# Optimization experiments

Hardware: AMD Instinct MI355X
Metric: run time of the kernel (lower is better)

The kernel has to match this reference:

```python
import jax, jax.numpy as jnp
import numpy as np

B, R, C, H, W = 8, 4, 64, 128, 128
RF, E = 256, 8
C2 = 2 * C
K = 3


def setup_inputs() -> dict:
    key = jax.random.key(0)
    ks = jax.random.split(key, 8)
    return {
        "x": jax.random.normal(ks[0], (B, C, H, W), jnp.float32),
        "routing": jax.random.normal(ks[1], (B, R, RF), jnp.float32),
        # nn.Linear(routing_features, num_experts)
        "routing_W": jax.random.normal(ks[2], (RF, E), jnp.float32) * 0.05,
        "routing_b": jnp.zeros((E,), jnp.float32),
        # CondConv2d expert weights: (E, Cout, Cin, k, k)
        "W1": jax.random.normal(ks[3], (E, C2, C, K, K), jnp.float32) * 0.04,
        "prelu_a": jnp.float32(0.25),  # PReLU single shared parameter
        "W2": jax.random.normal(ks[4], (E, C, C2, K, K), jnp.float32) * 0.03,
        # self-routing Linear(2*in_features, num_experts)
        "sr_W": jax.random.normal(ks[5], (C2, E), jnp.float32) * 0.08,
        "sr_b": jnp.zeros((E,), jnp.float32),
        # conv_output: Conv2d(in_features, 1, kernel_size=1) with bias
        "Wout": jax.random.normal(ks[6], (1, C), jnp.float32) * 0.1,
        "bout": jnp.zeros((1,), jnp.float32),
    }


def _prelu(x, a):
    return jnp.where(x >= 0, x, a * x)


def _cond_conv(x, rw, Wexp):
    # x: (B,Cin,H,W); rw: (B,E); Wexp: (E,Cout,Cin,k,k)
    # per-sample mixed kernel, then per-sample conv (vmap over batch)
    w = jnp.einsum('be,eoikl->boikl', rw, Wexp)
    def one(xi, wi):
        return jax.lax.conv_general_dilated(
            xi[None], wi, window_strides=(1, 1), padding=[(1, 1), (1, 1)])[0]
    return jax.vmap(one)(x, w)


def reference(x, routing, routing_W, routing_b, W1, prelu_a, W2, sr_W, sr_b, Wout, bout):
    rw = jax.nn.sigmoid(routing @ routing_W + routing_b)  # (B,R,E)
    rw = jnp.transpose(rw, (1, 0, 2))                     # (R,B,E)

    def per_head(rw_r):
        xc = _prelu(_cond_conv(x, rw_r, W1), prelu_a)      # (B,C2,H,W)
        pooled = xc.mean(axis=(2, 3))                      # adaptive_avg_pool2d(.,1)
        srw = pooled @ sr_W + sr_b                         # no sigmoid (per source)
        xc2 = _prelu(_cond_conv(xc, srw, W2), prelu_a)     # (B,C,H,W)
        out = jnp.einsum('bchw,oc->bohw', xc2, Wout)       # 1x1 conv
        return out + bout[None, :, None, None]             # (B,1,H,W)

    res = jax.vmap(per_head)(rw)                           # (R,B,1,H,W)
    return jnp.transpose(res[:, :, 0], (1, 0, 2, 3))       # (B,R,H,W)
```

## Files before the change

### kernel.cpp

```cpp
#include <hip/hip_runtime.h>
#include <stdint.h>


typedef _Float16 f16_t;
typedef _Float16 f16x8 __attribute__((ext_vector_type(8)));
typedef _Float16 f16x4 __attribute__((ext_vector_type(4)));
typedef float    f32x4 __attribute__((ext_vector_type(4)));

#define B_   8
#define R_   4
#define C_   64
#define C2_  128
#define H_   128
#define W_   128
#define E_   8
#define RF_  256
#define WP_  130
#define HP_  130

__device__ __forceinline__ f32x4 mfma16(f16x8 a, f16x8 b, f32x4 c) {
  return __builtin_amdgcn_mfma_f32_16x16x32_f16(a, b, c, 0, 0, 0);
}

__device__ __forceinline__ void gl16(const f16_t* g, f16_t* l) {
  __builtin_amdgcn_global_load_lds(
      (const __attribute__((address_space(1))) unsigned int*)(const void*)g,
      (__attribute__((address_space(3))) unsigned int*)(void*)l, 16, 0, 0);
}

__device__ __host__ __forceinline__ int sig(int n) { return (n ^ (n >> 2)) & 3; }

__global__ void k_rw(const float* __restrict__ routing, const float* __restrict__ rW,
                     const float* __restrict__ rB, float* __restrict__ rw,
                     float* __restrict__ pooled4) {
  int t = threadIdx.x;
  #pragma unroll
  for (int i = 0; i < 16; ++i) pooled4[i*256 + t] = 0.f;
  int e = t & 7, b = (t >> 3) & 7, r = t >> 6;
  float acc = rB[e];
  for (int f = 0; f < RF_; ++f)
    acc += routing[(b*R_ + r)*RF_ + f] * rW[f*E_ + e];
  rw[(r*B_ + b)*E_ + e] = 1.0f / (1.0f + __expf(-acc));
}

__global__ void k_zero(f16_t* __restrict__ xbt, f16_t* __restrict__ xct,
                       size_t xct_stride) {
  const f16x8 z = {0,0,0,0,0,0,0,0};
  int t = blockIdx.x*256 + threadIdx.x;
  if (t < 16640) {
    int ch = t & 7, u = t >> 3;
    int pix = u % 130; u /= 130;
    int rs = u & 1, b = u >> 1;
    *(f16x8*)&xbt[((size_t)(b*HP_ + rs*129)*WP_ + pix)*C_ + ch*8] = z;
    return;
  }
  t -= 16640;
  if (t < 133120) {
    int ch = t & 15, u = t >> 4;
    int pix = u % 130; u /= 130;
    int rs = u & 1; u >>= 1;
    int b = u & 7, r = u >> 3;
    *(f16x8*)&xct[(size_t)r*xct_stride + ((size_t)(b*HP_ + rs*129)*WP_ + pix)*C2_ + ch*8] = z;
    return;
  }
  t -= 133120;
  if (t < 131072) {
    int ch = t & 15, u = t >> 4;
    int hp = (u & 127) + 1; u >>= 7;
    int cs = u & 1; u >>= 1;
    int b = u & 7, r = u >> 3;
    *(f16x8*)&xct[(size_t)r*xct_stride + ((size_t)(b*HP_ + hp)*WP_ + cs*129)*C2_ + ch*8] = z;
  }
}

__global__ void k_xt(const float* __restrict__ x, f16_t* __restrict__ xbt) {
  int wh = blockIdx.x, h = blockIdx.y, b = blockIdx.z;
  int t = threadIdx.x;
  int w0 = wh * 64;
  __shared__ float tile[64][65];
  #pragma unroll
  for (int rep = 0; rep < 16; ++rep) {
    int idx = rep*256 + t;
    int c = idx >> 6, w = idx & 63;
    tile[c][w] = x[((size_t)(b*C_ + c)*H_ + h)*W_ + w0 + w];
  }
  __syncthreads();
  #pragma unroll
  for (int rep = 0; rep < 16; ++rep) {
    int idx = rep*256 + t;
    int w = idx >> 6, c = idx & 63;
    xbt[((size_t)(b*HP_ + h + 1)*WP_ + (w0 + w + 1))*C_ + c] = (f16_t)tile[c][w];
  }
  if (t < 64) {
    if (wh == 0) xbt[((size_t)(b*HP_ + h + 1)*WP_ + 0)*C_ + t]   = (f16_t)0.0f;
    else         xbt[((size_t)(b*HP_ + h + 1)*WP_ + 129)*C_ + t] = (f16_t)0.0f;
  }
}

__global__ void k_mix1(const float* __restrict__ rw, const float* __restrict__ W1,
                       f16_t* __restrict__ w1m) {
  int gid = blockIdx.x*256 + threadIdx.x;
  int cq4 = gid & 15;
  int s   = (gid >> 4) % 9;
  int t2  = (gid >> 4) / 9;
  int co  = t2 & 127;
  int rb  = t2 >> 7;
  float o0=0.f,o1=0.f,o2=0.f,o3=0.f;
  #pragma unroll
  for (int e = 0; e < E_; ++e) {
    float rv = rw[rb*E_ + e];
    const float* wp = W1 + (size_t)((e*C2_ + co)*C_ + cq4*4)*9 + s;
    o0 += rv*wp[0]; o1 += rv*wp[9]; o2 += rv*wp[18]; o3 += rv*wp[27];
  }
  f16x4 pk; pk[0]=(f16_t)o0; pk[1]=(f16_t)o1; pk[2]=(f16_t)o2; pk[3]=(f16_t)o3;
  int coh = co >> 6, co6 = co & 63;
  int cb  = cq4 >> 3;
  int cqu = (cq4 >> 1) & 3;
  int off = (cq4 & 1) * 4;
  size_t row = ((size_t)(rb*2 + coh)*2 + cb)*64 + co6;
  *(f16x4*)&w1m[row*288 + (size_t)(s*4 + (cqu ^ sig(co6)))*8 + off] = pk;
}

__global__ void k_mix2(const float* __restrict__ pooled, const float* __restrict__ srW,
                       const float* __restrict__ srb, const float* __restrict__ W2,
                       f16_t* __restrict__ w2m, size_t w2m_stride, int r0) {
  const int r = r0 + blockIdx.y;
  const float* pooled_r = pooled + (size_t)r*B_*C2_;
  f16_t* w2m_r = w2m + (size_t)r*w2m_stride;
  __shared__ float sw[64];
  int t = threadIdx.x;
  if (t < 64) {
    int b = t >> 3, e = t & 7;
    float acc = srb[e];
    for (int c = 0; c < C2_; ++c)
      acc += pooled_r[b*C2_ + c] * (1.0f/16384.0f) * srW[c*E_ + e];
    sw[t] = acc;
  }
  __syncthreads();
  int gid = blockIdx.x*256 + t;
  int c2q = gid & 31;
  int s   = (gid >> 5) % 9;
  int t2  = (gid >> 5) / 9;
  int co  = t2 & 63;
  int b   = t2 >> 6;
  float o0=0.f,o1=0.f,o2=0.f,o3=0.f;
  #pragma unroll
  for (int e = 0; e < E_; ++e) {
    float rv = sw[b*E_ + e];
    const float* wp = W2 + (size_t)((e*C_ + co)*C2_ + c2q*4)*9 + s;
    o0 += rv*wp[0]; o1 += rv*wp[9]; o2 += rv*wp[18]; o3 += rv*wp[27];
  }
  f16x4 pk; pk[0]=(f16_t)o0; pk[1]=(f16_t)o1; pk[2]=(f16_t)o2; pk[3]=(f16_t)o3;
  int it  = c2q >> 3;
  int cqu = (c2q >> 1) & 3;
  int off = (c2q & 1) * 4;
  size_t row = ((size_t)b*4 + it)*64 + co;
  *(f16x4*)&w2m_r[row*288 + (size_t)(s*4 + (cqu ^ sig(co)))*8 + off] = pk;
}

__global__ __launch_bounds__(256, 2) void k_conv1(
    const f16_t* __restrict__ xbt, const f16_t* __restrict__ w1m,
    const float* __restrict__ pa, f16_t* __restrict__ xct, size_t xct_stride,
    float* __restrict__ pooled, int r0)
{
  const int bx = blockIdx.x;
  const int b = bx & 7, h0 = (bx >> 3) << 1;
  const int coh = blockIdx.y;
  const int r = r0 + blockIdx.z;
  f16_t* xct_r = xct + (size_t)r*xct_stride;
  float* pooled_r = pooled + (size_t)r*B_*C2_;
  const int tid = threadIdx.x;
  const int lane = tid & 63;
  const int wid = tid >> 6;
  const int wrow = wid >> 1, wph = wid & 1;
  const int l15 = lane & 15, l4 = lane >> 4;
  __shared__ __align__(16) f16_t lA[64*288];
  __shared__ __align__(16) f16_t lB[2080*8];

  const int xorA = (l4 ^ sig(l15)) << 4;
  int bbase[3];
  #pragma unroll
  for (int dw = 0; dw < 3; ++dw) {
    int P0 = wph*64 + dw + l15;
    bbase[dw] = P0*64 + ((l4 ^ sig(P0)) << 4);
  }

  const f32x4 vzero = {0.f,0.f,0.f,0.f};
  f32x4 acc[4][4];
  #pragma unroll
  for (int i=0;i<4;++i)
    #pragma unroll
    for (int j=0;j<4;++j) acc[i][j] = vzero;

  const int rb = r*B_ + b;
  const f16_t* w1base = w1m + ((size_t)(rb*2 + coh)*2)*64*288;
  const f16_t* xb = xbt + ((size_t)(b*HP_ + h0))*WP_*C_;

  for (int cb = 0; cb < 2; ++cb) {
    __syncthreads();
    #pragma unroll
    for (int k = 0; k < 9; ++k) {
      int u = k*256 + tid;
      gl16(w1base + (size_t)cb*64*288 + (size_t)u*8, &lA[u*8]);
    }
    #pragma unroll
    for (int k = 0; k < 8; ++k) {
      int u = k*256 + tid;
      int row = u / 520, rem = u - row*520;
      int pix = rem >> 2, cq = (rem & 3) ^ sig(pix);
      gl16(xb + ((size_t)row*WP_ + pix)*C_ + cb*32 + cq*8, &lB[u*8]);
    }
    if (tid < 32) {
      int u = 2048 + tid;
      int rem = u - 1560;
      int pix = rem >> 2, cq = (rem & 3) ^ sig(pix);
      gl16(xb + ((size_t)3*WP_ + pix)*C_ + cb*32 + cq*8, &lB[u*8]);
    }
    __syncthreads();
    __builtin_amdgcn_s_setprio(1);
    #pragma unroll
    for (int dh = 0; dh < 3; ++dh) {
      #pragma unroll
      for (int dw = 0; dw < 3; ++dw) {
        const int s = dh*3 + dw;
        f16x8 af[4], bf[4];
        #pragma unroll
        for (int fm = 0; fm < 4; ++fm)
          af[fm] = *(const f16x8*)((const char*)lA + (fm*16 + l15)*576 + s*64 + xorA);
        #pragma unroll
        for (int fn = 0; fn < 4; ++fn)
          bf[fn] = *(const f16x8*)((const char*)lB + (wrow + dh)*8320 + bbase[dw] + fn*1024);
        #pragma unroll
        for (int fm = 0; fm < 4; ++fm)
          #pragma unroll
          for (int fn = 0; fn < 4; ++fn)
            acc[fm][fn] = mfma16(af[fm], bf[fn], acc[fm][fn]);
      }
    }
    __builtin_amdgcn_s_setprio(0);
  }

  const float a = pa[0];
  float ps[4][4];
  #pragma unroll
  for (int fm=0;fm<4;++fm)
    #pragma unroll
    for (int j=0;j<4;++j) ps[fm][j] = 0.f;
  #pragma unroll
  for (int fm = 0; fm < 4; ++fm)
    #pragma unroll
    for (int fn = 0; fn < 4; ++fn)
      #pragma unroll
      for (int j = 0; j < 4; ++j) {
        float v = acc[fm][fn][j];
        v = (v >= 0.f) ? v : a*v;
        acc[fm][fn][j] = v;
        ps[fm][j] += v;
      }
  #pragma unroll
  for (int fm = 0; fm < 4; ++fm)
    #pragma unroll
    for (int j = 0; j < 4; ++j) {
      float s = ps[fm][j];
      s += __shfl_xor(s, 1, 64);
      s += __shfl_xor(s, 2, 64);
      s += __shfl_xor(s, 4, 64);
      s += __shfl_xor(s, 8, 64);
      ps[fm][j] = s;
    }
  __syncthreads();
  f16_t* lso = lA;
  float* lps = (float*)lB;
  const int prow = wrow*128 + wph*64;
  #pragma unroll
  for (int fm = 0; fm < 4; ++fm)
    #pragma unroll
    for (int fn = 0; fn < 4; ++fn) {
      f16x4 pk;
      #pragma unroll
      for (int j = 0; j < 4; ++j) pk[j] = (f16_t)acc[fm][fn][j];
      *(f16x4*)&lso[(prow + fn*16 + l15)*72 + fm*16 + l4*4] = pk;
    }
  if (l15 == 0) {
    #pragma unroll
    for (int fm = 0; fm < 4; ++fm)
      #pragma unroll
      for (int j = 0; j < 4; ++j)
        lps[wid*64 + fm*16 + l4*4 + j] = ps[fm][j];
  }
  __syncthreads();
  #pragma unroll
  for (int p = 0; p < 8; ++p) {
    int i = p*256 + tid;
    int pl = i >> 3, q = i & 7;
    int row = pl >> 7, pix = pl & 127;
    uint4 v = *(const uint4*)&lso[pl*72 + q*8];
    *(uint4*)(xct_r + ((size_t)(b*HP_ + h0 + row + 1)*WP_ + pix + 1)*C2_ + coh*64 + q*8) = v;
  }
  if (tid < 64) {
    float s = lps[tid] + lps[64 + tid] + lps[128 + tid] + lps[192 + tid];
    atomicAdd(&pooled_r[b*C2_ + coh*64 + tid], s);
  }
}

__global__ __launch_bounds__(256, 2) void k_conv2(
    const f16_t* __restrict__ xct, size_t xct_stride,
    const f16_t* __restrict__ w2m, size_t w2m_stride,
    const float* __restrict__ pa, const float* __restrict__ Wout,
    const float* __restrict__ bout, float* __restrict__ out, int r0)
{
  const int bx = blockIdx.x;
  const int b = bx & 7, h0 = (bx >> 3) << 1;
  const int r = r0 + blockIdx.y;
  const int tid = threadIdx.x;
  const int lane = tid & 63;
  const int wid = tid >> 6;
  const int wrow = wid >> 1, wph = wid & 1;
  const int l15 = lane & 15, l4 = lane >> 4;
  __shared__ __align__(16) f16_t lA[64*288];
  __shared__ __align__(16) f16_t lB[2080*8];

  const int xorA = (l4 ^ sig(l15)) << 4;
  int bbase[3];
  #pragma unroll
  for (int dw = 0; dw < 3; ++dw) {
    int P0 = wph*64 + dw + l15;
    bbase[dw] = P0*64 + ((l4 ^ sig(P0)) << 4);
  }

  const f32x4 vzero = {0.f,0.f,0.f,0.f};
  f32x4 acc[4][4];
  #pragma unroll
  for (int i=0;i<4;++i)
    #pragma unroll
    for (int j=0;j<4;++j) acc[i][j] = vzero;

  const f16_t* w2base = w2m + (size_t)r*w2m_stride + (size_t)b*4*64*288;
  const f16_t* xb = xct + (size_t)r*xct_stride + ((size_t)(b*HP_ + h0))*WP_*C2_;

  for (int it = 0; it < 4; ++it) {
    __syncthreads();
    #pragma unroll
    for (int k = 0; k < 9; ++k) {
      int u = k*256 + tid;
      gl16(w2base + (size_t)it*64*288 + (size_t)u*8, &lA[u*8]);
    }
    #pragma unroll
    for (int k = 0; k < 8; ++k) {
      int u = k*256 + tid;
      int row = u / 520, rem = u - row*520;
      int pix = rem >> 2, cq = (rem & 3) ^ sig(pix);
      gl16(xb + ((size_t)row*WP_ + pix)*C2_ + it*32 + cq*8, &lB[u*8]);
    }
    if (tid < 32) {
      int u = 2048 + tid;
      int rem = u - 1560;
      int pix = rem >> 2, cq = (rem & 3) ^ sig(pix);
      gl16(xb + ((size_t)3*WP_ + pix)*C2_ + it*32 + cq*8, &lB[u*8]);
    }
    __syncthreads();
    __builtin_amdgcn_s_setprio(1);
    #pragma unroll
    for (int dh = 0; dh < 3; ++dh) {
      #pragma unroll
      for (int dw = 0; dw < 3; ++dw) {
        const int s = dh*3 + dw;
        f16x8 af[4], bf[4];
        #pragma unroll
        for (int fm = 0; fm < 4; ++fm)
          af[fm] = *(const f16x8*)((const char*)lA + (fm*16 + l15)*576 + s*64 + xorA);
        #pragma unroll
        for (int fn = 0; fn < 4; ++fn)
          bf[fn] = *(const f16x8*)((const char*)lB + (wrow + dh)*8320 + bbase[dw] + fn*1024);
        #pragma unroll
        for (int fm = 0; fm < 4; ++fm)
          #pragma unroll
          for (int fn = 0; fn < 4; ++fn)
            acc[fm][fn] = mfma16(af[fm], bf[fn], acc[fm][fn]);
      }
    }
    __builtin_amdgcn_s_setprio(0);
  }

  const float a  = pa[0];
  const float bo = bout[0];
  float wr_[4][4];
  #pragma unroll
  for (int fm = 0; fm < 4; ++fm)
    #pragma unroll
    for (int j = 0; j < 4; ++j)
      wr_[fm][j] = Wout[fm*16 + l4*4 + j];
  float* orow = out + ((size_t)((b*R_ + r)*H_ + h0 + wrow))*W_;
  #pragma unroll
  for (int fn = 0; fn < 4; ++fn) {
    float s = 0.f;
    #pragma unroll
    for (int fm = 0; fm < 4; ++fm)
      #pragma unroll
      for (int j = 0; j < 4; ++j) {
        float v = acc[fm][fn][j];
        v = (v >= 0.f) ? v : a*v;
        s += wr_[fm][j]*v;
      }
    s += __shfl_xor(s, 16, 64);
    s += __shfl_xor(s, 32, 64);
    if (lane < 16)
      orow[wph*64 + fn*16 + lane] = s + bo;
  }
}

extern "C" void kernel_launch(void* const* d_in, const int* in_sizes, int n_in,
                              void* d_out, int out_size, void* d_ws, size_t ws_size,
                              hipStream_t stream) {
  (void)in_sizes; (void)n_in; (void)out_size;
  const float* x       = (const float*)d_in[0];
  const float* routing = (const float*)d_in[1];
  const float* rW      = (const float*)d_in[2];
  const float* rB      = (const float*)d_in[3];
  const float* W1      = (const float*)d_in[4];
  const float* pa      = (const float*)d_in[5];
  const float* W2      = (const float*)d_in[6];
  const float* srW     = (const float*)d_in[7];
  const float* srb     = (const float*)d_in[8];
  const float* Wout    = (const float*)d_in[9];
  const float* bout    = (const float*)d_in[10];
  float* out = (float*)d_out;

  const size_t xct_one = (size_t)B_*HP_*WP_*C2_;
  const size_t w2m_one = (size_t)2048*288;
  const size_t need_fused = 17305600ull + 4718592ull + 4*xct_one*2 + 4*w2m_one*2 + 32768ull;
  const bool fused = (ws_size >= need_fused);
  const int ncopies = fused ? 4 : 1;
  const size_t xs = fused ? xct_one : 0;
  const size_t ws2 = fused ? w2m_one : 0;

  char* ws = (char*)d_ws;
  size_t off = 0;
  f16_t* xbt = (f16_t*)(ws + off); off += (size_t)B_*HP_*WP_*C_*2;
  f16_t* w1m = (f16_t*)(ws + off); off += (size_t)8192*288*2;
  f16_t* xct = (f16_t*)(ws + off); off += xct_one*2*ncopies;
  f16_t* w2m = (f16_t*)(ws + off); off += w2m_one*2*ncopies;
  float* rw     = (float*)(ws + off); off += (size_t)R_*B_*E_*4;
  float* pooled = (float*)(ws + off); off += (size_t)R_*B_*C2_*4;

  k_rw  <<<1, 256, 0, stream>>>(routing, rW, rB, rw, pooled);
  k_zero<<<1097, 256, 0, stream>>>(xbt, xct, xs);
  k_xt  <<<dim3(2, H_, B_), 256, 0, stream>>>(x, xbt);
  k_mix1<<<2304, 256, 0, stream>>>(rw, W1, w1m);
  if (fused) {
    k_conv1<<<dim3(512, 2, 4), 256, 0, stream>>>(xbt, w1m, pa, xct, xs, pooled, 0);
    k_mix2 <<<dim3(576, 4), 256, 0, stream>>>(pooled, srW, srb, W2, w2m, ws2, 0);
    k_conv2<<<dim3(512, 4), 256, 0, stream>>>(xct, xs, w2m, ws2, pa, Wout, bout, out, 0);
  } else {
    for (int r = 0; r < R_; ++r) {
      k_conv1<<<dim3(512, 2, 1), 256, 0, stream>>>(xbt, w1m, pa, xct, xs, pooled, r);
      k_mix2 <<<dim3(576, 1), 256, 0, stream>>>(pooled, srW, srb, W2, w2m, ws2, r);
      k_conv2<<<dim3(512, 1), 256, 0, stream>>>(xct, xs, w2m, ws2, pa, Wout, bout, out, r);
    }
  }
}
```

Before: 242.8 us.

## Switch activations to channel-group-planar layout and enlarge conv tiles to 8 rows

Activations and mixed weights now use an 8-channel-unit, channel-group-major layout instead of pixel-major with an XOR swizzle. Each conv block covers 8 output rows with 512 threads, so the haloed input tile is reused across more rows. Weights are streamed per tap into a double buffer that is prefetched while the MFMAs run, and conv2 prefetches the next channel block into registers. The cost is a barrier after every tap, larger LDS use that limits occupancy, more pooled atomics, and a serialized staged store of the conv1 output.

```diff
diff --git a/kernel.cpp b/kernel.cpp
--- a/kernel.cpp
+++ b/kernel.cpp
@@ -15,8 +15,8 @@
 #define W_   128
 #define E_   8
 #define RF_  256
+#define HP_  130
 #define WP_  130
-#define HP_  130
 
 __device__ __forceinline__ f32x4 mfma16(f16x8 a, f16x8 b, f32x4 c) {
   return __builtin_amdgcn_mfma_f32_16x16x32_f16(a, b, c, 0, 0, 0);
@@ -27,8 +27,6 @@
       (const __attribute__((address_space(1))) unsigned int*)(const void*)g,
       (__attribute__((address_space(3))) unsigned int*)(void*)l, 16, 0, 0);
 }
-
-__device__ __host__ __forceinline__ int sig(int n) { return (n ^ (n >> 2)) & 3; }
 
 __global__ void k_rw(const float* __restrict__ routing, const float* __restrict__ rW,
                      const float* __restrict__ rB, float* __restrict__ rw,
@@ -44,32 +42,27 @@
 }
 
 __global__ void k_zero(f16_t* __restrict__ xbt, f16_t* __restrict__ xct,
-                       size_t xct_stride) {
+                       size_t xsu) {
   const f16x8 z = {0,0,0,0,0,0,0,0};
   int t = blockIdx.x*256 + threadIdx.x;
   if (t < 16640) {
-    int ch = t & 7, u = t >> 3;
-    int pix = u % 130; u /= 130;
-    int rs = u & 1, b = u >> 1;
-    *(f16x8*)&xbt[((size_t)(b*HP_ + rs*129)*WP_ + pix)*C_ + ch*8] = z;
+    int un = t % 1040, q = t / 1040;
+    int rs = q & 1, b = q >> 1;
+    *(f16x8*)&xbt[((size_t)(b*HP_ + rs*129)*1040 + un)*8] = z;
     return;
   }
   t -= 16640;
   if (t < 133120) {
-    int ch = t & 15, u = t >> 4;
-    int pix = u % 130; u /= 130;
-    int rs = u & 1; u >>= 1;
-    int b = u & 7, r = u >> 3;
-    *(f16x8*)&xct[(size_t)r*xct_stride + ((size_t)(b*HP_ + rs*129)*WP_ + pix)*C2_ + ch*8] = z;
+    int un = t % 2080, q = t / 2080;
+    int rs = q & 1, b = (q >> 1) & 7, r = q >> 4;
+    *(f16x8*)&xct[((size_t)r*xsu + (size_t)(b*HP_ + rs*129)*2080 + un)*8] = z;
     return;
   }
   t -= 133120;
   if (t < 131072) {
-    int ch = t & 15, u = t >> 4;
-    int hp = (u & 127) + 1; u >>= 7;
-    int cs = u & 1; u >>= 1;
-    int b = u & 7, r = u >> 3;
-    *(f16x8*)&xct[(size_t)r*xct_stride + ((size_t)(b*HP_ + hp)*WP_ + cs*129)*C2_ + ch*8] = z;
+    int cs = t & 1, u = (t >> 1) & 15, prow = ((t >> 5) & 127) + 1;
+    int b = (t >> 12) & 7, r = t >> 15;
+    *(f16x8*)&xct[((size_t)r*xsu + (size_t)(b*HP_ + prow)*2080 + u*130 + cs*129)*8] = z;
   }
 }
 
@@ -85,15 +78,17 @@
     tile[c][w] = x[((size_t)(b*C_ + c)*H_ + h)*W_ + w0 + w];
   }
   __syncthreads();
+  size_t rowb = (size_t)(b*HP_ + h + 1)*1040;
   #pragma unroll
   for (int rep = 0; rep < 16; ++rep) {
     int idx = rep*256 + t;
     int w = idx >> 6, c = idx & 63;
-    xbt[((size_t)(b*HP_ + h + 1)*WP_ + (w0 + w + 1))*C_ + c] = (f16_t)tile[c][w];
+    xbt[(rowb + (c>>3)*130 + (w0 + w + 1))*8 + (c & 7)] = (f16_t)tile[c][w];
   }
   if (t < 64) {
-    if (wh == 0) xbt[((size_t)(b*HP_ + h + 1)*WP_ + 0)*C_ + t]   = (f16_t)0.0f;
-    else         xbt[((size_t)(b*HP_ + h + 1)*WP_ + 129)*C_ + t] = (f16_t)0.0f;
+    int u = t >> 3, c7 = t & 7;
+    int gp = (wh == 0) ? 0 : 129;
+    xbt[(rowb + u*130 + gp)*8 + c7] = (f16_t)0.0f;
   }
 }
 
@@ -114,19 +109,17 @@
   }
   f16x4 pk; pk[0]=(f16_t)o0; pk[1]=(f16_t)o1; pk[2]=(f16_t)o2; pk[3]=(f16_t)o3;
   int coh = co >> 6, co6 = co & 63;
-  int cb  = cq4 >> 3;
-  int cqu = (cq4 >> 1) & 3;
-  int off = (cq4 & 1) * 4;
-  size_t row = ((size_t)(rb*2 + coh)*2 + cb)*64 + co6;
-  *(f16x4*)&w1m[row*288 + (size_t)(s*4 + (cqu ^ sig(co6)))*8 + off] = pk;
+  int cb = cq4 >> 3, u2 = (cq4 >> 1) & 3, half = cq4 & 1;
+  size_t unit = ((size_t)(((rb*2 + coh)*2 + cb)*9 + s)*4 + u2)*64 + co6;
+  *(f16x4*)&w1m[unit*8 + half*4] = pk;
 }
 
 __global__ void k_mix2(const float* __restrict__ pooled, const float* __restrict__ srW,
                        const float* __restrict__ srb, const float* __restrict__ W2,
-                       f16_t* __restrict__ w2m, size_t w2m_stride, int r0) {
+                       f16_t* __restrict__ w2m, int r0) {
   const int r = r0 + blockIdx.y;
   const float* pooled_r = pooled + (size_t)r*B_*C2_;
-  f16_t* w2m_r = w2m + (size_t)r*w2m_stride;
+  f16_t* w2m_r = w2m + (size_t)r*73728*8;
   __shared__ float sw[64];
   int t = threadIdx.x;
   if (t < 64) {
@@ -151,93 +144,87 @@
     o0 += rv*wp[0]; o1 += rv*wp[9]; o2 += rv*wp[18]; o3 += rv*wp[27];
   }
   f16x4 pk; pk[0]=(f16_t)o0; pk[1]=(f16_t)o1; pk[2]=(f16_t)o2; pk[3]=(f16_t)o3;
-  int it  = c2q >> 3;
-  int cqu = (c2q >> 1) & 3;
-  int off = (c2q & 1) * 4;
-  size_t row = ((size_t)b*4 + it)*64 + co;
-  *(f16x4*)&w2m_r[row*288 + (size_t)(s*4 + (cqu ^ sig(co)))*8 + off] = pk;
-}
-
-__global__ __launch_bounds__(256, 2) void k_conv1(
+  int cb = c2q >> 3, u2 = (c2q >> 1) & 3, half = c2q & 1;
+  size_t unit = ((size_t)((b*4 + cb)*9 + s)*4 + u2)*64 + co;
+  *(f16x4*)&w2m_r[unit*8 + half*4] = pk;
+}
+
+__global__ __launch_bounds__(512, 2) void k_conv1(
     const f16_t* __restrict__ xbt, const f16_t* __restrict__ w1m,
-    const float* __restrict__ pa, f16_t* __restrict__ xct, size_t xct_stride,
+    const float* __restrict__ pa, f16_t* __restrict__ xct, size_t xsu,
     float* __restrict__ pooled, int r0)
 {
   const int bx = blockIdx.x;
-  const int b = bx & 7, h0 = (bx >> 3) << 1;
+  const int b = bx & 7, h0 = (bx >> 3) << 3;
   const int coh = blockIdx.y;
   const int r = r0 + blockIdx.z;
-  f16_t* xct_r = xct + (size_t)r*xct_stride;
-  float* pooled_r = pooled + (size_t)r*B_*C2_;
   const int tid = threadIdx.x;
   const int lane = tid & 63;
   const int wid = tid >> 6;
-  const int wrow = wid >> 1, wph = wid & 1;
   const int l15 = lane & 15, l4 = lane >> 4;
-  __shared__ __align__(16) f16_t lA[64*288];
-  __shared__ __align__(16) f16_t lB[2080*8];
-
-  const int xorA = (l4 ^ sig(l15)) << 4;
-  int bbase[3];
-  #pragma unroll
-  for (int dw = 0; dw < 3; ++dw) {
-    int P0 = wph*64 + dw + l15;
-    bbase[dw] = P0*64 + ((l4 ^ sig(P0)) << 4);
-  }
-
-  const f32x4 vzero = {0.f,0.f,0.f,0.f};
-  f32x4 acc[4][4];
+  __shared__ __align__(16) f16_t lB[5200*8];
+  __shared__ __align__(16) f16_t lA[2][256*8];
+
+  f32x4 acc[4][8];
   #pragma unroll
   for (int i=0;i<4;++i)
     #pragma unroll
-    for (int j=0;j<4;++j) acc[i][j] = vzero;
-
-  const int rb = r*B_ + b;
-  const f16_t* w1base = w1m + ((size_t)(rb*2 + coh)*2)*64*288;
-  const f16_t* xb = xbt + ((size_t)(b*HP_ + h0))*WP_*C_;
-
+    for (int j=0;j<8;++j) acc[i][j] = (f32x4){0.f,0.f,0.f,0.f};
+
+  const f16_t* xsrc  = xbt + ((size_t)(b*HP_ + h0))*1040*8;
+  const f16_t* wbase = w1m + ((size_t)((r*B_ + b)*2 + coh))*2*9*256*8;
+  f16_t* xct_r = xct + (size_t)blockIdx.z*xsu*8;
+
+  #pragma unroll
+  for (int k = 0; k < 10; ++k) {
+    int u = tid + 512*k; int lr = u/520, j = u - lr*520;
+    gl16(xsrc + ((size_t)(lr*1040 + j))*8, &lB[u*8]);
+  }
+  if (tid < 80) {
+    int u = 5120 + tid; int lr = u/520, j = u - lr*520;
+    gl16(xsrc + ((size_t)(lr*1040 + j))*8, &lB[u*8]);
+  }
+  if (tid < 256) gl16(wbase + (size_t)tid*8, &lA[0][tid*8]);
+  __syncthreads();
+
+  int cur = 0;
   for (int cb = 0; cb < 2; ++cb) {
-    __syncthreads();
-    #pragma unroll
-    for (int k = 0; k < 9; ++k) {
-      int u = k*256 + tid;
-      gl16(w1base + (size_t)cb*64*288 + (size_t)u*8, &lA[u*8]);
-    }
-    #pragma unroll
-    for (int k = 0; k < 8; ++k) {
-      int u = k*256 + tid;
-      int row = u / 520, rem = u - row*520;
-      int pix = rem >> 2, cq = (rem & 3) ^ sig(pix);
-      gl16(xb + ((size_t)row*WP_ + pix)*C_ + cb*32 + cq*8, &lB[u*8]);
-    }
-    if (tid < 32) {
-      int u = 2048 + tid;
-      int rem = u - 1560;
-      int pix = rem >> 2, cq = (rem & 3) ^ sig(pix);
-      gl16(xb + ((size_t)3*WP_ + pix)*C_ + cb*32 + cq*8, &lB[u*8]);
-    }
-    __syncthreads();
-    __builtin_amdgcn_s_setprio(1);
-    #pragma unroll
-    for (int dh = 0; dh < 3; ++dh) {
-      #pragma unroll
-      for (int dw = 0; dw < 3; ++dw) {
-        const int s = dh*3 + dw;
-        f16x8 af[4], bf[4];
+    if (cb) {
+      #pragma unroll
+      for (int k = 0; k < 10; ++k) {
+        int u = tid + 512*k; int lr = u/520, j = u - lr*520;
+        gl16(xsrc + ((size_t)(lr*1040 + 520 + j))*8, &lB[u*8]);
+      }
+      if (tid < 80) {
+        int u = 5120 + tid; int lr = u/520, j = u - lr*520;
+        gl16(xsrc + ((size_t)(lr*1040 + 520 + j))*8, &lB[u*8]);
+      }
+      __syncthreads();
+    }
+    #pragma unroll
+    for (int s = 0; s < 9; ++s) {
+      const int nc = (s < 8) ? cb : cb + 1;
+      const int ns = (s < 8) ? s + 1 : 0;
+      if (nc < 2 && tid < 256)
+        gl16(wbase + ((size_t)((nc*9 + ns)*256 + tid))*8, &lA[cur^1][tid*8]);
+      const int dh = s / 3, dw = s % 3;
+      f16x8 af[4], bf[8];
+      #pragma unroll
+      for (int fm = 0; fm < 4; ++fm)
+        af[fm] = *(const f16x8*)&lA[cur][(l4*64 + fm*16 + l15)*8];
+      #pragma unroll
+      for (int fn = 0; fn < 8; ++fn)
+        bf[fn] = *(const f16x8*)&lB[((wid + dh)*520 + l4*130 + fn*16 + l15 + dw)*8];
+      __builtin_amdgcn_s_setprio(1);
+      #pragma unroll
+      for (int fm = 0; fm < 4; ++fm)
         #pragma unroll
-        for (int fm = 0; fm < 4; ++fm)
-          af[fm] = *(const f16x8*)((const char*)lA + (fm*16 + l15)*576 + s*64 + xorA);
-        #pragma unroll
-        for (int fn = 0; fn < 4; ++fn)
-          bf[fn] = *(const f16x8*)((const char*)lB + (wrow + dh)*8320 + bbase[dw] + fn*1024);
-        #pragma unroll
-        for (int fm = 0; fm < 4; ++fm)
-          #pragma unroll
-          for (int fn = 0; fn < 4; ++fn)
-            acc[fm][fn] = mfma16(af[fm], bf[fn], acc[fm][fn]);
-      }
-    }
-    __builtin_amdgcn_s_setprio(0);
+        for (int fn = 0; fn < 8; ++fn)
+          acc[fm][fn] = mfma16(af[fm], bf[fn], acc[fm][fn]);
+      __builtin_amdgcn_s_setprio(0);
+      __syncthreads();
+      cur ^= 1;
+    }
   }
 
   const float a = pa[0];
@@ -249,7 +236,7 @@
   #pragma unroll
   for (int fm = 0; fm < 4; ++fm)
     #pragma unroll
-    for (int fn = 0; fn < 4; ++fn)
+    for (int fn = 0; fn < 8; ++fn)
       #pragma unroll
       for (int j = 0; j < 4; ++j) {
         float v = acc[fm][fn][j];
@@ -266,120 +253,119 @@
       s += __shfl_xor(s, 2, 64);
       s += __shfl_xor(s, 4, 64);
       s += __shfl_xor(s, 8, 64);
-      ps[fm][j] = s;
-    }
-  __syncthreads();
-  f16_t* lso = lA;
-  float* lps = (float*)lB;
-  const int prow = wrow*128 + wph*64;
-  #pragma unroll
-  for (int fm = 0; fm < 4; ++fm)
-    #pragma unroll
-    for (int fn = 0; fn < 4; ++fn) {
-      f16x4 pk;
-      #pragma unroll
-      for (int j = 0; j < 4; ++j) pk[j] = (f16_t)acc[fm][fn][j];
-      *(f16x4*)&lso[(prow + fn*16 + l15)*72 + fm*16 + l4*4] = pk;
-    }
-  if (l15 == 0) {
-    #pragma unroll
-    for (int fm = 0; fm < 4; ++fm)
-      #pragma unroll
-      for (int j = 0; j < 4; ++j)
-        lps[wid*64 + fm*16 + l4*4 + j] = ps[fm][j];
-  }
-  __syncthreads();
-  #pragma unroll
-  for (int p = 0; p < 8; ++p) {
-    int i = p*256 + tid;
-    int pl = i >> 3, q = i & 7;
-    int row = pl >> 7, pix = pl & 127;
-    uint4 v = *(const uint4*)&lso[pl*72 + q*8];
-    *(uint4*)(xct_r + ((size_t)(b*HP_ + h0 + row + 1)*WP_ + pix + 1)*C2_ + coh*64 + q*8) = v;
-  }
-  if (tid < 64) {
-    float s = lps[tid] + lps[64 + tid] + lps[128 + tid] + lps[192 + tid];
-    atomicAdd(&pooled_r[b*C2_ + coh*64 + tid], s);
-  }
-}
-
-__global__ __launch_bounds__(256, 2) void k_conv2(
-    const f16_t* __restrict__ xct, size_t xct_stride,
-    const f16_t* __restrict__ w2m, size_t w2m_stride,
+      if (l15 == 0)
+        atomicAdd(&pooled[(size_t)r*B_*C2_ + b*C2_ + coh*64 + fm*16 + l4*4 + j], s);
+    }
+  #pragma unroll
+  for (int t4 = 0; t4 < 4; ++t4) {
+    if ((wid >> 1) == t4) {
+      const int rr = wid & 1;
+      #pragma unroll
+      for (int fm = 0; fm < 4; ++fm)
+        #pragma unroll
+        for (int fn = 0; fn < 8; ++fn) {
+          f16x4 pk;
+          #pragma unroll
+          for (int j = 0; j < 4; ++j) pk[j] = (f16_t)acc[fm][fn][j];
+          int pix = fn*16 + l15;
+          int cof = (fm*16 + l4*4) ^ ((pix & 7) << 3);
+          *(f16x4*)&lB[(rr*128 + pix)*64 + cof] = pk;
+        }
+    }
+    __syncthreads();
+    #pragma unroll
+    for (int k = 0; k < 4; ++k) {
+      int idx = tid + 512*k;
+      int rr = idx >> 10, u = (idx >> 7) & 7, pix = idx & 127;
+      f16x8 v = *(const f16x8*)&lB[(rr*128 + pix)*64 + ((u ^ (pix & 7)) << 3)];
+      size_t gu = (size_t)(b*HP_ + h0 + 2*t4 + rr + 1)*2080 + (coh*8 + u)*130 + pix + 1;
+      *(f16x8*)(xct_r + gu*8) = v;
+    }
+    __syncthreads();
+  }
+}
+
+__global__ __launch_bounds__(512, 2) void k_conv2(
+    const f16_t* __restrict__ xct, size_t xsu,
+    const f16_t* __restrict__ w2m,
     const float* __restrict__ pa, const float* __restrict__ Wout,
     const float* __restrict__ bout, float* __restrict__ out, int r0)
 {
   const int bx = blockIdx.x;
-  const int b = bx & 7, h0 = (bx >> 3) << 1;
+  const int b = bx & 7, h0 = (bx >> 3) << 3;
   const int r = r0 + blockIdx.y;
   const int tid = threadIdx.x;
   const int lane = tid & 63;
   const int wid = tid >> 6;
-  const int wrow = wid >> 1, wph = wid & 1;
   const int l15 = lane & 15, l4 = lane >> 4;
-  __shared__ __align__(16) f16_t lA[64*288];
-  __shared__ __align__(16) f16_t lB[2080*8];
-
-  const int xorA = (l4 ^ sig(l15)) << 4;
-  int bbase[3];
-  #pragma unroll
-  for (int dw = 0; dw < 3; ++dw) {
-    int P0 = wph*64 + dw + l15;
-    bbase[dw] = P0*64 + ((l4 ^ sig(P0)) << 4);
-  }
-
-  const f32x4 vzero = {0.f,0.f,0.f,0.f};
-  f32x4 acc[4][4];
+  __shared__ __align__(16) f16_t lB[5200*8];
+  __shared__ __align__(16) f16_t lA[2][256*8];
+
+  f32x4 acc[4][8];
   #pragma unroll
   for (int i=0;i<4;++i)
     #pragma unroll
-    for (int j=0;j<4;++j) acc[i][j] = vzero;
-
-  const f16_t* w2base = w2m + (size_t)r*w2m_stride + (size_t)b*4*64*288;
-  const f16_t* xb = xct + (size_t)r*xct_stride + ((size_t)(b*HP_ + h0))*WP_*C2_;
-
-  for (int it = 0; it < 4; ++it) {
-    __syncthreads();
-    #pragma unroll
-    for (int k = 0; k < 9; ++k) {
-      int u = k*256 + tid;
-      gl16(w2base + (size_t)it*64*288 + (size_t)u*8, &lA[u*8]);
-    }
-    #pragma unroll
-    for (int k = 0; k < 8; ++k) {
-      int u = k*256 + tid;
-      int row = u / 520, rem = u - row*520;
-      int pix = rem >> 2, cq = (rem & 3) ^ sig(pix);
-      gl16(xb + ((size_t)row*WP_ + pix)*C2_ + it*32 + cq*8, &lB[u*8]);
-    }
-    if (tid < 32) {
-      int u = 2048 + tid;
-      int rem = u - 1560;
-      int pix = rem >> 2, cq = (rem & 3) ^ sig(pix);
-      gl16(xb + ((size_t)3*WP_ + pix)*C2_ + it*32 + cq*8, &lB[u*8]);
-    }
-    __syncthreads();
-    __builtin_amdgcn_s_setprio(1);
-    #pragma unroll
-    for (int dh = 0; dh < 3; ++dh) {
-      #pragma unroll
-      for (int dw = 0; dw < 3; ++dw) {
-        const int s = dh*3 + dw;
-        f16x8 af[4], bf[4];
+    for (int j=0;j<8;++j) acc[i][j] = (f32x4){0.f,0.f,0.f,0.f};
+
+  const f16_t* xsrc  = xct + ((size_t)blockIdx.y*xsu + (size_t)(b*HP_ + h0)*2080)*8;
+  const f16_t* wbase = w2m + ((size_t)r*73728 + (size_t)b*4*9*256)*8;
+
+  #pragma unroll
+  for (int k = 0; k < 10; ++k) {
+    int u = tid + 512*k; int lr = u/520, j = u - lr*520;
+    gl16(xsrc + ((size_t)(lr*2080 + j))*8, &lB[u*8]);
+  }
+  if (tid < 80) {
+    int u = 5120 + tid; int lr = u/520, j = u - lr*520;
+    gl16(xsrc + ((size_t)(lr*2080 + j))*8, &lB[u*8]);
+  }
+  if (tid < 256) gl16(wbase + (size_t)tid*8, &lA[0][tid*8]);
+  __syncthreads();
+
+  int cur = 0;
+  uint4 br[11];
+  for (int cb = 0; cb < 4; ++cb) {
+    if (cb < 3) {
+      #pragma unroll
+      for (int k = 0; k < 10; ++k) {
+        int u = tid + 512*k; int lr = u/520, j = u - lr*520;
+        br[k] = *(const uint4*)(xsrc + ((size_t)(lr*2080 + (cb+1)*520 + j))*8);
+      }
+      if (tid < 80) {
+        int u = 5120 + tid; int lr = u/520, j = u - lr*520;
+        br[10] = *(const uint4*)(xsrc + ((size_t)(lr*2080 + (cb+1)*520 + j))*8);
+      }
+    }
+    #pragma unroll
+    for (int s = 0; s < 9; ++s) {
+      const int nc = (s < 8) ? cb : cb + 1;
+      const int ns = (s < 8) ? s + 1 : 0;
+      if (nc < 4 && tid < 256)
+        gl16(wbase + ((size_t)((nc*9 + ns)*256 + tid))*8, &lA[cur^1][tid*8]);
+      const int dh = s / 3, dw = s % 3;
+      f16x8 af[4], bf[8];
+      #pragma unroll
+      for (int fm = 0; fm < 4; ++fm)
+        af[fm] = *(const f16x8*)&lA[cur][(l4*64 + fm*16 + l15)*8];
+      #pragma unroll
+      for (int fn = 0; fn < 8; ++fn)
+        bf[fn] = *(const f16x8*)&lB[((wid + dh)*520 + l4*130 + fn*16 + l15 + dw)*8];
+      __builtin_amdgcn_s_setprio(1);
+      #pragma unroll
+      for (int fm = 0; fm < 4; ++fm)
         #pragma unroll
-        for (int fm = 0; fm < 4; ++fm)
-          af[fm] = *(const f16x8*)((const char*)lA + (fm*16 + l15)*576 + s*64 + xorA);
-        #pragma unroll
-        for (int fn = 0; fn < 4; ++fn)
-          bf[fn] = *(const f16x8*)((const char*)lB + (wrow + dh)*8320 + bbase[dw] + fn*1024);
-        #pragma unroll
-        for (int fm = 0; fm < 4; ++fm)
-          #pragma unroll
-          for (int fn = 0; fn < 4; ++fn)
-            acc[fm][fn] = mfma16(af[fm], bf[fn], acc[fm][fn]);
-      }
-    }
-    __builtin_amdgcn_s_setprio(0);
+        for (int fn = 0; fn < 8; ++fn)
+          acc[fm][fn] = mfma16(af[fm], bf[fn], acc[fm][fn]);
+      __builtin_amdgcn_s_setprio(0);
+      __syncthreads();
+      cur ^= 1;
+    }
+    if (cb < 3) {
+      #pragma unroll
+      for (int k = 0; k < 10; ++k) { int u = tid + 512*k; *(uint4*)&lB[u*8] = br[k]; }
+      if (tid < 80)                { int u = 5120 + tid;  *(uint4*)&lB[u*8] = br[10]; }
+      __syncthreads();
+    }
   }
 
   const float a  = pa[0];
@@ -390,9 +376,9 @@
     #pragma unroll
     for (int j = 0; j < 4; ++j)
       wr_[fm][j] = Wout[fm*16 + l4*4 + j];
-  float* orow = out + ((size_t)((b*R_ + r)*H_ + h0 + wrow))*W_;
-  #pragma unroll
-  for (int fn = 0; fn < 4; ++fn) {
+  float* orow = out + ((size_t)((b*R_ + r)*H_ + h0 + wid))*W_;
+  #pragma unroll
+  for (int fn = 0; fn < 8; ++fn) {
     float s = 0.f;
     #pragma unroll
     for (int fm = 0; fm < 4; ++fm)
@@ -405,7 +391,7 @@
     s += __shfl_xor(s, 16, 64);
     s += __shfl_xor(s, 32, 64);
     if (lane < 16)
-      orow[wph*64 + fn*16 + lane] = s + bo;
+      orow[fn*16 + lane] = s + bo;
   }
 }
 
@@ -426,36 +412,38 @@
   const float* bout    = (const float*)d_in[10];
   float* out = (float*)d_out;
 
-  const size_t xct_one = (size_t)B_*HP_*WP_*C2_;
-  const size_t w2m_one = (size_t)2048*288;
-  const size_t need_fused = 17305600ull + 4718592ull + 4*xct_one*2 + 4*w2m_one*2 + 32768ull;
+  const size_t xbt_b = (size_t)B_*HP_*1040*16;
+  const size_t w1m_b = (size_t)294912*16;
+  const size_t xct_u = (size_t)B_*HP_*2080;
+  const size_t xct_b = xct_u*16;
+  const size_t w2m_b = (size_t)4*73728*16;
+  const size_t need_fused = xbt_b + w1m_b + 4*xct_b + w2m_b + 32768;
   const bool fused = (ws_size >= need_fused);
   const int ncopies = fused ? 4 : 1;
-  const size_t xs = fused ? xct_one : 0;
-  const size_t ws2 = fused ? w2m_one : 0;
+  const size_t xsu = fused ? xct_u : 0;
 
   char* ws = (char*)d_ws;
   size_t off = 0;
-  f16_t* xbt = (f16_t*)(ws + off); off += (size_t)B_*HP_*WP_*C_*2;
-  f16_t* w1m = (f16_t*)(ws + off); off += (size_t)8192*288*2;
-  f16_t* xct = (f16_t*)(ws + off); off += xct_one*2*ncopies;
-  f16_t* w2m = (f16_t*)(ws + off); off += w2m_one*2*ncopies;
+  f16_t* xbt = (f16_t*)(ws + off); off += xbt_b;
+  f16_t* w1m = (f16_t*)(ws + off); off += w1m_b;
+  f16_t* xct = (f16_t*)(ws + off); off += xct_b*ncopies;
+  f16_t* w2m = (f16_t*)(ws + off); off += w2m_b;
   float* rw     = (float*)(ws + off); off += (size_t)R_*B_*E_*4;
   float* pooled = (float*)(ws + off); off += (size_t)R_*B_*C2_*4;
 
   k_rw  <<<1, 256, 0, stream>>>(routing, rW, rB, rw, pooled);
-  k_zero<<<1097, 256, 0, stream>>>(xbt, xct, xs);
+  k_zero<<<1097, 256, 0, stream>>>(xbt, xct, xsu);
   k_xt  <<<dim3(2, H_, B_), 256, 0, stream>>>(x, xbt);
   k_mix1<<<2304, 256, 0, stream>>>(rw, W1, w1m);
   if (fused) {
-    k_conv1<<<dim3(512, 2, 4), 256, 0, stream>>>(xbt, w1m, pa, xct, xs, pooled, 0);
-    k_mix2 <<<dim3(576, 4), 256, 0, stream>>>(pooled, srW, srb, W2, w2m, ws2, 0);
-    k_conv2<<<dim3(512, 4), 256, 0, stream>>>(xct, xs, w2m, ws2, pa, Wout, bout, out, 0);
+    k_conv1<<<dim3(128, 2, 4), 512, 0, stream>>>(xbt, w1m, pa, xct, xsu, pooled, 0);
+    k_mix2 <<<dim3(576, 4), 256, 0, stream>>>(pooled, srW, srb, W2, w2m, 0);
+    k_conv2<<<dim3(128, 4), 512, 0, stream>>>(xct, xsu, w2m, pa, Wout, bout, out, 0);
   } else {
     for (int r = 0; r < R_; ++r) {
-      k_conv1<<<dim3(512, 2, 1), 256, 0, stream>>>(xbt, w1m, pa, xct, xs, pooled, r);
-      k_mix2 <<<dim3(576, 1), 256, 0, stream>>>(pooled, srW, srb, W2, w2m, ws2, r);
-      k_conv2<<<dim3(512, 1), 256, 0, stream>>>(xct, xs, w2m, ws2, pa, Wout, bout, out, r);
-    }
-  }
-}
+      k_conv1<<<dim3(128, 2, 1), 512, 0, stream>>>(xbt, w1m, pa, xct, 0, pooled, r);
+      k_mix2 <<<dim3(576, 1), 256, 0, stream>>>(pooled, srW, srb, W2, w2m, r);
+      k_conv2<<<dim3(128, 1), 512, 0, stream>>>(xct, 0, w2m, pa, Wout, bout, out, r);
+    }
+  }
+}
```

New measurement: 394.0 us. +62.2%, slower.

## Prefetch next K-chunk into registers during MFMA compute in both conv kernels

Applied to the files above, without the earlier changes.

Both conv kernels now load the first weight and activation chunk into LDS before the loop. For each later chunk, the data is fetched into registers (uint4 arrays) while the current chunk's MFMAs run, then written to LDS between barriers. This overlaps global-memory latency with matrix math instead of stalling at each chunk boundary. The cost is about 18 extra 128-bit registers per thread, which may reduce occupancy or cause spills given the 64-float accumulator tile.

```diff
diff --git a/kernel.cpp b/kernel.cpp
--- a/kernel.cpp
+++ b/kernel.cpp
@@ -185,38 +185,53 @@
     bbase[dw] = P0*64 + ((l4 ^ sig(P0)) << 4);
   }
 
-  const f32x4 vzero = {0.f,0.f,0.f,0.f};
   f32x4 acc[4][4];
   #pragma unroll
   for (int i=0;i<4;++i)
     #pragma unroll
-    for (int j=0;j<4;++j) acc[i][j] = vzero;
+    for (int j=0;j<4;++j) acc[i][j] = (f32x4){0.f,0.f,0.f,0.f};
 
   const int rb = r*B_ + b;
   const f16_t* w1base = w1m + ((size_t)(rb*2 + coh)*2)*64*288;
   const f16_t* xb = xbt + ((size_t)(b*HP_ + h0))*WP_*C_;
 
+  int brow[8], bpsw[8], trow = 3, tpsw = 0;
+  #pragma unroll
+  for (int k = 0; k < 8; ++k) {
+    int u = k*256 + tid;
+    int row = u / 520, rem = u - row*520;
+    int pix = rem >> 2, cq = (rem & 3) ^ sig(pix);
+    brow[k] = row; bpsw[k] = pix*C_ + cq*8;
+  }
+  {
+    int u = 2048 + (tid & 31);
+    int rem = u - 1560;
+    int pix = rem >> 2, cq = (rem & 3) ^ sig(pix);
+    tpsw = pix*C_ + cq*8;
+  }
+
+  #pragma unroll
+  for (int k = 0; k < 9; ++k)
+    gl16(w1base + (size_t)(k*256 + tid)*8, &lA[(k*256 + tid)*8]);
+  #pragma unroll
+  for (int k = 0; k < 8; ++k)
+    gl16(xb + (size_t)brow[k]*WP_*C_ + bpsw[k], &lB[(k*256 + tid)*8]);
+  if (tid < 32)
+    gl16(xb + (size_t)trow*WP_*C_ + 0*32 + tpsw, &lB[(2048 + tid)*8]);
+  __syncthreads();
+
+  uint4 ar[9], br[8], bt = {0,0,0,0};
   for (int cb = 0; cb < 2; ++cb) {
-    __syncthreads();
-    #pragma unroll
-    for (int k = 0; k < 9; ++k) {
-      int u = k*256 + tid;
-      gl16(w1base + (size_t)cb*64*288 + (size_t)u*8, &lA[u*8]);
-    }
-    #pragma unroll
-    for (int k = 0; k < 8; ++k) {
-      int u = k*256 + tid;
-      int row = u / 520, rem = u - row*520;
-      int pix = rem >> 2, cq = (rem & 3) ^ sig(pix);
-      gl16(xb + ((size_t)row*WP_ + pix)*C_ + cb*32 + cq*8, &lB[u*8]);
-    }
-    if (tid < 32) {
-      int u = 2048 + tid;
-      int rem = u - 1560;
-      int pix = rem >> 2, cq = (rem & 3) ^ sig(pix);
-      gl16(xb + ((size_t)3*WP_ + pix)*C_ + cb*32 + cq*8, &lB[u*8]);
-    }
-    __syncthreads();
+    if (cb == 0) {
+      #pragma unroll
+      for (int k = 0; k < 9; ++k)
+        ar[k] = *(const uint4*)(w1base + (size_t)64*288 + (size_t)(k*256 + tid)*8);
+      #pragma unroll
+      for (int k = 0; k < 8; ++k)
+        br[k] = *(const uint4*)(xb + (size_t)brow[k]*WP_*C_ + 32 + bpsw[k]);
+      if (tid < 32)
+        bt = *(const uint4*)(xb + (size_t)trow*WP_*C_ + 32 + tpsw);
+    }
     __builtin_amdgcn_s_setprio(1);
     #pragma unroll
     for (int dh = 0; dh < 3; ++dh) {
@@ -238,6 +253,15 @@
       }
     }
     __builtin_amdgcn_s_setprio(0);
+    if (cb == 0) {
+      __syncthreads();
+      #pragma unroll
+      for (int k = 0; k < 9; ++k) *(uint4*)&lA[(k*256 + tid)*8] = ar[k];
+      #pragma unroll
+      for (int k = 0; k < 8; ++k) *(uint4*)&lB[(k*256 + tid)*8] = br[k];
+      if (tid < 32) *(uint4*)&lB[(2048 + tid)*8] = bt;
+      __syncthreads();
+    }
   }
 
   const float a = pa[0];
@@ -328,37 +352,52 @@
     bbase[dw] = P0*64 + ((l4 ^ sig(P0)) << 4);
   }
 
-  const f32x4 vzero = {0.f,0.f,0.f,0.f};
   f32x4 acc[4][4];
   #pragma unroll
   for (int i=0;i<4;++i)
     #pragma unroll
-    for (int j=0;j<4;++j) acc[i][j] = vzero;
+    for (int j=0;j<4;++j) acc[i][j] = (f32x4){0.f,0.f,0.f,0.f};
 
   const f16_t* w2base = w2m + (size_t)r*w2m_stride + (size_t)b*4*64*288;
   const f16_t* xb = xct + (size_t)r*xct_stride + ((size_t)(b*HP_ + h0))*WP_*C2_;
 
+  int brow[8], bpsw[8], tpsw = 0;
+  #pragma unroll
+  for (int k = 0; k < 8; ++k) {
+    int u = k*256 + tid;
+    int row = u / 520, rem = u - row*520;
+    int pix = rem >> 2, cq = (rem & 3) ^ sig(pix);
+    brow[k] = row; bpsw[k] = pix*C2_ + cq*8;
+  }
+  {
+    int u = 2048 + (tid & 31);
+    int rem = u - 1560;
+    int pix = rem >> 2, cq = (rem & 3) ^ sig(pix);
+    tpsw = pix*C2_ + cq*8;
+  }
+
+  #pragma unroll
+  for (int k = 0; k < 9; ++k)
+    gl16(w2base + (size_t)(k*256 + tid)*8, &lA[(k*256 + tid)*8]);
+  #pragma unroll
+  for (int k = 0; k < 8; ++k)
+    gl16(xb + (size_t)brow[k]*WP_*C2_ + bpsw[k], &lB[(k*256 + tid)*8]);
+  if (tid < 32)
+    gl16(xb + (size_t)3*WP_*C2_ + tpsw, &lB[(2048 + tid)*8]);
+  __syncthreads();
+
+  uint4 ar[9], br[8], bt = {0,0,0,0};
   for (int it = 0; it < 4; ++it) {
-    __syncthreads();
-    #pragma unroll
-    for (int k = 0; k < 9; ++k) {
-      int u = k*256 + tid;
-      gl16(w2base + (size_t)it*64*288 + (size_t)u*8, &lA[u*8]);
-    }
-    #pragma unroll
-    for (int k = 0; k < 8; ++k) {
-      int u = k*256 + tid;
-      int row = u / 520, rem = u - row*520;
-      int pix = rem >> 2, cq = (rem & 3) ^ sig(pix);
-      gl16(xb + ((size_t)row*WP_ + pix)*C2_ + it*32 + cq*8, &lB[u*8]);
-    }
-    if (tid < 32) {
-      int u = 2048 + tid;
-      int rem = u - 1560;
-      int pix = rem >> 2, cq = (rem & 3) ^ sig(pix);
-      gl16(xb + ((size_t)3*WP_ + pix)*C2_ + it*32 + cq*8, &lB[u*8]);
-    }
-    __syncthreads();
+    if (it < 3) {
+      #pragma unroll
+      for (int k = 0; k < 9; ++k)
+        ar[k] = *(const uint4*)(w2base + (size_t)(it+1)*64*288 + (size_t)(k*256 + tid)*8);
+      #pragma unroll
+      for (int k = 0; k < 8; ++k)
+        br[k] = *(const uint4*)(xb + (size_t)brow[k]*WP_*C2_ + (it+1)*32 + bpsw[k]);
+      if (tid < 32)
+        bt = *(const uint4*)(xb + (size_t)3*WP_*C2_ + (it+1)*32 + tpsw);
+    }
     __builtin_amdgcn_s_setprio(1);
     #pragma unroll
     for (int dh = 0; dh < 3; ++dh) {
@@ -380,6 +419,15 @@
       }
     }
     __builtin_amdgcn_s_setprio(0);
+    if (it < 3) {
+      __syncthreads();
+      #pragma unroll
+      for (int k = 0; k < 9; ++k) *(uint4*)&lA[(k*256 + tid)*8] = ar[k];
+      #pragma unroll
+      for (int k = 0; k < 8; ++k) *(uint4*)&lB[(k*256 + tid)*8] = br[k];
+      if (tid < 32) *(uint4*)&lB[(2048 + tid)*8] = bt;
+      __syncthreads();
+    }
   }
 
   const float a  = pa[0];
```

New measurement: 397.4 us. 63.6% more time.
